# Kernel optimization log

Measured on AMD Instinct MI355X. Metric: run time of the kernel, lower is better.

The kernel has to match this reference:

```python
import jax, jax.numpy as jnp
import numpy as np

N = 50000   # nodes
E = 800000  # edges
IN = 128    # in_channels
H = 256     # hidden_channels
G = 128     # graphs in batch
NEG_SLOPE = 0.2


def _gat_conv(x, src, dst, W, a_src, a_dst, b):
    # PyG GATConv, heads=1: xp = W x; e_ij = LeakyReLU(a_src.xp_j + a_dst.xp_i);
    # softmax over incoming edges of target i; out_i = sum_j alpha_ij xp_j + b
    xp = x @ W                                   # [N, H]
    e = jax.nn.leaky_relu(xp[src] @ a_src + xp[dst] @ a_dst, NEG_SLOPE)  # [Et]
    m = jax.ops.segment_max(e, dst, num_segments=N)
    m = jnp.where(jnp.isfinite(m), m, 0.0)
    p = jnp.exp(e - m[dst])
    denom = jax.ops.segment_sum(p, dst, num_segments=N)
    alpha = p / denom[dst]
    return jax.ops.segment_sum(alpha[:, None] * xp[src], dst, num_segments=N) + b


def _gru_step_h0(x, W_ih, W_hh, b_ih, b_hh):
    # torch.nn.GRU, seq_len=1, h0=0. Gate order: r, z, n.
    gi = x @ W_ih.T + b_ih                       # [N, 3H]
    i_r, i_z, i_n = jnp.split(gi, 3, axis=-1)
    h_r, h_z, h_n = jnp.split(b_hh, 3)           # h0=0 -> hidden gates are biases
    r = jax.nn.sigmoid(i_r + h_r)
    z = jax.nn.sigmoid(i_z + h_z)
    n = jnp.tanh(i_n + r * h_n)
    return (1.0 - z) * n                         # + z * h0 (=0)


def setup_inputs() -> dict:
    key = jax.random.key(0)
    ks = jax.random.split(key, 18)
    s = 0.05
    inp = {
        "x": jax.random.normal(ks[0], (N, IN), jnp.float32),
        "edge_index": jax.random.randint(ks[1], (2, E), 0, N, dtype=jnp.int32).astype(jnp.int64),
        "batch": jnp.sort(jax.random.randint(ks[2], (N,), 0, G, dtype=jnp.int32)).astype(jnp.int64),
        # GAT layer 0 (in->H) and layer 1 (H->H)
        "W0": jax.random.normal(ks[3], (IN, H), jnp.float32) * s,
        "a_src0": jax.random.normal(ks[4], (H,), jnp.float32) * s,
        "a_dst0": jax.random.normal(ks[5], (H,), jnp.float32) * s,
        "b0": jnp.zeros((H,), jnp.float32),
        "W1": jax.random.normal(ks[6], (H, H), jnp.float32) * s,
        "a_src1": jax.random.normal(ks[7], (H,), jnp.float32) * s,
        "a_dst1": jax.random.normal(ks[8], (H,), jnp.float32) * s,
        "b1": jnp.zeros((H,), jnp.float32),
        # GRU(H, H)
        "W_ih": jax.random.normal(ks[9], (3 * H, H), jnp.float32) * s,
        "W_hh": jax.random.normal(ks[10], (3 * H, H), jnp.float32) * s,
        "b_ih": jnp.zeros((3 * H,), jnp.float32),
        "b_hh": jnp.zeros((3 * H,), jnp.float32),
        # super_node_fc
        "Wf": jax.random.normal(ks[11], (H, H), jnp.float32) * s,
        "bf": jnp.zeros((H,), jnp.float32),
    }
    return inp


def reference(x, edge_index, batch, W0, a_src0, a_dst0, b0, W1, a_src1, a_dst1, b1,
              W_ih, W_hh, b_ih, b_hh, Wf, bf):
    # add self loops (PyG GATConv default)
    loops = jnp.arange(N, dtype=edge_index.dtype)
    src = jnp.concatenate([edge_index[0], loops])
    dst = jnp.concatenate([edge_index[1], loops])

    h = jax.nn.relu(_gat_conv(x, src, dst, W0, a_src0, a_dst0, b0))  # dropout=identity (eval)
    h = jax.nn.relu(_gat_conv(h, src, dst, W1, a_src1, a_dst1, b1))

    h = _gru_step_h0(h, W_ih, W_hh, b_ih, b_hh)                      # [N, H]

    h = jax.ops.segment_sum(h, batch, num_segments=G)                # global_add_pool [G, H]
    super_node = jnp.mean(h, axis=0, keepdims=True)                  # [1, H]
    super_node = jax.nn.relu(super_node @ Wf.T + bf)
    return jnp.concatenate([h, jnp.broadcast_to(super_node, (G, H))], axis=1)  # [G, 2H]
```

## Files before the change

kernel.cpp:

```cpp
#include <hip/hip_runtime.h>
#include <hip/hip_fp16.h>
#include <math.h>

#define N_NODES 50000
#define N_PAD   50176
#define N_EDGES 800000
#define ET (N_EDGES + N_NODES)
#define IN_CH 128
#define H 256
#define G_GRAPHS 128
#define NEG_SLOPE 0.2f
#define NB 391

typedef __attribute__((ext_vector_type(8))) short short8;
typedef __attribute__((ext_vector_type(4))) float f32x4;
typedef __attribute__((ext_vector_type(2))) float f32x2;
typedef unsigned short u16;
typedef unsigned char u8;


#if __has_builtin(__builtin_amdgcn_cvt_f32_fp8) && __has_builtin(__builtin_amdgcn_cvt_pk_fp8_f32)
#define USE_FP8_BUILTINS 1
#else
#define USE_FP8_BUILTINS 0
#endif
#if USE_FP8_BUILTINS && __has_builtin(__builtin_amdgcn_cvt_pk_f32_fp8)
#define HAVE_PK_DEC 1
#else
#define HAVE_PK_DEC 0
#endif

__device__ inline u16 f2bf(float v) {
    unsigned u = __float_as_uint(v);
    unsigned r = (u + 0x7FFFu + ((u >> 16) & 1u)) >> 16;
    return (u16)r;
}
__device__ inline float bf2f(u16 v) {
    return __uint_as_float(((unsigned)v) << 16);
}

#if USE_FP8_BUILTINS
#define FP8_WSCALE 1.0f
__device__ inline unsigned fp8_pack4(float a, float b, float c, float d) {
    int v = 0;
    v = __builtin_amdgcn_cvt_pk_fp8_f32(a, b, v, false);
    v = __builtin_amdgcn_cvt_pk_fp8_f32(c, d, v, true);
    return (unsigned)v;
}
__device__ inline void fp8_dec4(unsigned rv, float& f0, float& f1, float& f2, float& f3) {
#if HAVE_PK_DEC
    f32x2 lo = __builtin_amdgcn_cvt_pk_f32_fp8((int)rv, false);
    f32x2 hi = __builtin_amdgcn_cvt_pk_f32_fp8((int)rv, true);
    f0 = lo.x; f1 = lo.y; f2 = hi.x; f3 = hi.y;
#else
    f0 = __builtin_amdgcn_cvt_f32_fp8((int)rv, 0);
    f1 = __builtin_amdgcn_cvt_f32_fp8((int)rv, 1);
    f2 = __builtin_amdgcn_cvt_f32_fp8((int)rv, 2);
    f3 = __builtin_amdgcn_cvt_f32_fp8((int)rv, 3);
#endif
}
#else
#define FP8_WSCALE 256.0f
__device__ inline u8 fp8_enc1(float f) {
    unsigned u = __float_as_uint(f);
    unsigned s = (u >> 31) << 7;
    float a = fabsf(f);
    if (a >= 448.f) return (u8)(s | 0x7E);
    unsigned bits = __float_as_uint(a);
    int exp = (int)((bits >> 23) & 255) - 127;
    unsigned m23 = bits & 0x7fffff;
    if (exp < -6) {
        int m = (int)rintf(a * 512.f);
        if (m >= 8) return (u8)(s | (1 << 3));
        return (u8)(s | m);
    }
    int e8 = exp + 7;
    unsigned m = m23 >> 20, rem = m23 & 0xFFFFF;
    if (rem > 0x80000 || (rem == 0x80000 && (m & 1))) m++;
    if (m == 8) { m = 0; e8++; }
    if (e8 > 15 || (e8 == 15 && m == 7)) return (u8)(s | 0x7E);
    return (u8)(s | (e8 << 3) | m);
}
__device__ inline unsigned fp8_pack4(float a, float b, float c, float d) {
    return (unsigned)fp8_enc1(a) | ((unsigned)fp8_enc1(b) << 8) |
           ((unsigned)fp8_enc1(c) << 16) | ((unsigned)fp8_enc1(d) << 24);
}
__device__ inline void fp8_dec4(unsigned rv, float& f0, float& f1, float& f2, float& f3) {
    unsigned hA = ((rv & 0x00800080u) << 8) | ((rv & 0x007f007fu) << 7);
    unsigned rs = rv >> 8;
    unsigned hB = ((rs & 0x00800080u) << 8) | ((rs & 0x007f007fu) << 7);
    __half2 a = *(__half2*)&hA;
    __half2 b = *(__half2*)&hB;
    f0 = __low2float(a);  f2 = __high2float(a);
    f1 = __low2float(b);  f3 = __high2float(b);
}
#endif

__device__ inline void async_cp16(const u16* g, u16* l) {
    __builtin_amdgcn_global_load_lds(
        (const __attribute__((address_space(1))) unsigned int*)g,
        (__attribute__((address_space(3))) unsigned int*)l,
        16, 0, 0);
}

__global__ __launch_bounds__(256) void bucket_hist(const int* __restrict__ ei,
                                                   int* __restrict__ gcnt) {
    __shared__ int h[NB];
    int t = threadIdx.x;
    for (int b = t; b < NB; b += 256) h[b] = 0;
    __syncthreads();
    for (int e = blockIdx.x * 256 + t; e < N_EDGES; e += gridDim.x * 256)
        atomicAdd(&h[ei[N_EDGES + e] >> 7], 1);
    __syncthreads();
    for (int b = t; b < NB; b += 256)
        if (h[b]) atomicAdd(&gcnt[b], h[b]);
}

__global__ __launch_bounds__(512) void bucket_scan(const int* __restrict__ gcnt,
                                                   int* __restrict__ off,
                                                   int* __restrict__ cur) {
    __shared__ int s[NB + 1];
    int t = threadIdx.x;
    if (t < NB) s[t] = gcnt[t];
    __syncthreads();
    if (t == 0) {
        int a = 0;
        for (int b = 0; b < NB; b++) { int c = s[b]; s[b] = a; a += c; }
        s[NB] = a;
    }
    __syncthreads();
    if (t <= NB) { off[t] = s[t]; if (t < NB) cur[t] = s[t]; }
}

#define EPT 16
__global__ __launch_bounds__(256) void bucket_scatter(const int* __restrict__ ei,
                                                      int* __restrict__ bucketCur,
                                                      int2* __restrict__ rec) {
    __shared__ int cnt[NB];
    __shared__ int base[NB];
    int t = threadIdx.x;
    for (int b = t; b < NB; b += 256) cnt[b] = 0;
    __syncthreads();
    int e0 = blockIdx.x * (256 * EPT);
    int sa[EPT], da[EPT], rk[EPT];
#pragma unroll
    for (int k = 0; k < EPT; k++) {
        int e = e0 + k * 256 + t;
        if (e < N_EDGES) {
            sa[k] = ei[e];
            da[k] = ei[N_EDGES + e];
            rk[k] = atomicAdd(&cnt[da[k] >> 7], 1);
        }
    }
    __syncthreads();
    for (int b = t; b < NB; b += 256) {
        int c = cnt[b];
        base[b] = c ? atomicAdd(&bucketCur[b], c) : 0;
    }
    __syncthreads();
#pragma unroll
    for (int k = 0; k < EPT; k++) {
        int e = e0 + k * 256 + t;
        if (e < N_EDGES) rec[base[da[k] >> 7] + rk[k]] = make_int2(sa[k], da[k]);
    }
}

__global__ __launch_bounds__(256) void build_csr(const int2* __restrict__ rec,
                                                 const int* __restrict__ off,
                                                 int* __restrict__ indptr,
                                                 int* __restrict__ eidsSrc) {
    __shared__ int cnt[128];
    __shared__ int scn[128];
    __shared__ int cur[128];
    int b = blockIdx.x, t = threadIdx.x;
    int nInB = N_NODES - b * 128;
    if (nInB > 128) nInB = 128;
    if (t < 128) cnt[t] = 0;
    __syncthreads();
    int lo = off[b], hi = off[b + 1];
    for (int i = lo + t; i < hi; i += 256) atomicAdd(&cnt[rec[i].y & 127], 1);
    __syncthreads();
    if (t < 128) scn[t] = cnt[t] + 1;
    __syncthreads();
    for (int o = 1; o < 128; o <<= 1) {
        int v = 0;
        if (t < 128 && t >= o) v = scn[t - o];
        __syncthreads();
        if (t < 128 && t >= o) scn[t] += v;
        __syncthreads();
    }
    int base = off[b] + 128 * b;
    if (t < nInB) {
        int start = base + (t ? scn[t - 1] : 0);
        int node = b * 128 + t;
        indptr[node] = start;
        eidsSrc[start] = node;
        cur[t] = start + 1;
    }
    if (b == 0 && t == 0) indptr[N_NODES] = ET;
    __syncthreads();
    for (int i = lo + t; i < hi; i += 256) {
        int2 r = rec[i];
        int pos = atomicAdd(&cur[r.y & 127], 1);
        eidsSrc[pos] = r.x;
    }
}

__global__ __launch_bounds__(256) void prep_kernel(const float* __restrict__ x,
                                                   const float* __restrict__ Wih,
                                                   const float* __restrict__ W0,
                                                   const float* __restrict__ W1,
                                                   const float* __restrict__ b0,
                                                   const float* __restrict__ b1,
                                                   u16* __restrict__ x_bf,
                                                   u16* __restrict__ Wih_bf,
                                                   u16* __restrict__ W0t,
                                                   u16* __restrict__ W1t,
                                                   float* __restrict__ b0p,
                                                   float* __restrict__ b1p) {
    int i = blockIdx.x * 256 + threadIdx.x;
    int seg = blockIdx.y;
    if (seg == 0) {
        if (i < N_NODES * IN_CH / 4) {
            float4 v = *(const float4*)&x[i * 4];
            ushort4 o = {f2bf(v.x), f2bf(v.y), f2bf(v.z), f2bf(v.w)};
            *(ushort4*)&x_bf[i * 4] = o;
        }
    } else if (seg == 1) {
        if (i < 3 * H * H) {
            int r = i >> 8, p = i & 255;
            int c = ((p & 15) << 4) | (p >> 4);
            Wih_bf[(size_t)r * H + p] = f2bf(Wih[(size_t)r * H + c]);
        }
    } else if (seg == 2) {
        if (i < IN_CH * H) {
            int k = i / H, n = i % H;
            W0t[(size_t)n * IN_CH + k] = f2bf(W0[i]);
        }
    } else if (seg == 3) {
        if (i < H * H) {
            int n = i >> 8, p = i & 255;
            int c = ((p & 15) << 4) | (p >> 4);
            W1t[(size_t)n * H + p] = f2bf(W1[(size_t)c * H + n]);
        }
    } else {
        if (i < H) {
            int c = ((i & 15) << 4) | (i >> 4);
            b0p[i] = b0[c];
            b1p[i] = b1[c];
        }
    }
}

template <bool FUSE>
__global__ __launch_bounds__(256, 2) void gemm_wide(const u16* __restrict__ A,
                                                    const u16* __restrict__ Bt,
                                                    u16* __restrict__ C,
                                                    u8* __restrict__ C8,
                                                    const float* __restrict__ avS,
                                                    const float* __restrict__ avD,
                                                    float* __restrict__ sS,
                                                    float* __restrict__ sD,
                                                    int M, int K, int Ntot) {
    __shared__ u16 As[128][32];
    __shared__ u16 Bs[256][32];
    __shared__ float rSp[2][128];
    __shared__ float rDp[2][128];
    int t = threadIdx.x;
    int m0 = blockIdx.x * 128;
    int n0 = blockIdx.y * 256;
    int wave = t >> 6, lane = t & 63;
    int wm = (wave >> 1) * 64, wn = (wave & 1) * 128;
    int lrow = lane & 15;
    int lq = lane >> 4;

    f32x4 acc[4][8];
#pragma unroll
    for (int i = 0; i < 4; i++)
#pragma unroll
        for (int j = 0; j < 8; j++)
            acc[i][j] = (f32x4){0.f, 0.f, 0.f, 0.f};

    int r0 = t >> 2;
    int qs = (t & 3) ^ ((t >> 3) & 3);
    const u16* gA0 = A + (size_t)(m0 + r0) * K + qs * 8;
    const u16* gA1 = gA0 + (size_t)64 * K;
    const u16* gB0 = Bt + (size_t)(n0 + r0) * K + qs * 8;
    const u16* gB1 = gB0 + (size_t)64 * K;
    const u16* gB2 = gB0 + (size_t)128 * K;
    const u16* gB3 = gB0 + (size_t)192 * K;
    u16* lA0 = &As[0][0] + t * 8;
    u16* lA1 = lA0 + 256 * 8;
    u16* lB0 = &Bs[0][0] + t * 8;
    u16* lB1 = lB0 + 256 * 8;
    u16* lB2 = lB0 + 512 * 8;
    u16* lB3 = lB0 + 768 * 8;

    int swz8 = (lq ^ ((lrow >> 1) & 3)) * 8;

    for (int k0 = 0; k0 < K; k0 += 32) {
        __syncthreads();
        async_cp16(gA0 + k0, lA0);
        async_cp16(gA1 + k0, lA1);
        async_cp16(gB0 + k0, lB0);
        async_cp16(gB1 + k0, lB1);
        async_cp16(gB2 + k0, lB2);
        async_cp16(gB3 + k0, lB3);
        __syncthreads();
        short8 af[4], bfr[8];
#pragma unroll
        for (int i = 0; i < 4; i++)
            af[i] = *(const short8*)&As[wm + i * 16 + lrow][swz8];
#pragma unroll
        for (int j = 0; j < 8; j++)
            bfr[j] = *(const short8*)&Bs[wn + j * 16 + lrow][swz8];
#pragma unroll
        for (int i = 0; i < 4; i++)
#pragma unroll
            for (int j = 0; j < 8; j++)
                acc[i][j] = __builtin_amdgcn_mfma_f32_16x16x32_bf16(af[i], bfr[j], acc[i][j], 0, 0, 0);
    }

    if constexpr (FUSE) {
        float aS[8], aD[8];
#pragma unroll
        for (int j = 0; j < 8; j++) {
            aS[j] = avS[wn + j * 16 + lrow];
            aD[j] = avD[wn + j * 16 + lrow];
        }
        int woff = wn ? 8 : 0;
#pragma unroll
        for (int i = 0; i < 4; i++) {
#pragma unroll
            for (int reg = 0; reg < 4; reg++) {
                float ps = 0.f, pd = 0.f;
#pragma unroll
                for (int j = 0; j < 8; j++) {
                    float v = acc[i][j][reg];
                    ps += v * aS[j];
                    pd += v * aD[j];
                }
                uint2 pk;
                pk.x = fp8_pack4(acc[i][0][reg], acc[i][1][reg], acc[i][2][reg], acc[i][3][reg]);
                pk.y = fp8_pack4(acc[i][4][reg], acc[i][5][reg], acc[i][6][reg], acc[i][7][reg]);
                int row = m0 + wm + i * 16 + lq * 4 + reg;
                *(uint2*)&C8[(size_t)row * 256 + lrow * 16 + woff] = pk;
#pragma unroll
                for (int msk = 1; msk < 16; msk <<= 1) {
                    ps += __shfl_xor(ps, msk);
                    pd += __shfl_xor(pd, msk);
                }
                if (lrow == 0) {
                    int lr = wm + i * 16 + lq * 4 + reg;
                    rSp[wave & 1][lr] = ps;
                    rDp[wave & 1][lr] = pd;
                }
            }
        }
        __syncthreads();
        if (t < 128) {
            int gm = m0 + t;
            if (gm < M) {
                sS[gm] = rSp[0][t] + rSp[1][t];
                sD[gm] = rDp[0][t] + rDp[1][t];
            }
        }
    } else {
#pragma unroll
        for (int i = 0; i < 4; i++) {
#pragma unroll
            for (int reg = 0; reg < 4; reg++) {
                int gm = m0 + wm + i * 16 + lq * 4 + reg;
                if (gm < M) {
#pragma unroll
                    for (int j = 0; j < 8; j++) {
                        int gn = n0 + wn + j * 16 + lrow;
                        C[(size_t)gm * Ntot + gn] = f2bf(acc[i][j][reg]);
                    }
                }
            }
        }
    }
}

__global__ __launch_bounds__(256) void gat_agg_fp8(const u8* __restrict__ xp8,
                                                   const float* __restrict__ s_src,
                                                   const float* __restrict__ s_dst,
                                                   const int* __restrict__ indptr,
                                                   const int* __restrict__ eidsSrc,
                                                   const float* __restrict__ bias,
                                                   u16* __restrict__ out) {
    __shared__ int2 sSW[4][64];
    int wave = threadIdx.x >> 6, lane = threadIdx.x & 63;
    int n = blockIdx.x * 4 + wave;
    int start = indptr[n];
    int deg = indptr[n + 1] - start;
    float sdn = s_dst[n];
    int col = lane << 2;
    float a0 = 0.f, a1 = 0.f, a2 = 0.f, a3 = 0.f;

    if (deg <= 64) {
        int s = 0;
        float v = -1e30f;
        if (lane < deg) {
            s = eidsSrc[start + lane];
            float u = s_src[s] + sdn;
            v = (u >= 0.f) ? u : NEG_SLOPE * u;
        }
        float m = v;
#pragma unroll
        for (int off = 32; off; off >>= 1) m = fmaxf(m, __shfl_xor(m, off));
        float pw = (lane < deg) ? expf(v - m) : 0.f;
        float dsum = pw;
#pragma unroll
        for (int off = 32; off; off >>= 1) dsum += __shfl_xor(dsum, off);
        float w = pw * (FP8_WSCALE / dsum);
        sSW[wave][lane] = make_int2(s * H, __float_as_int(w));
        int j = 0;
        for (; j + 16 <= deg; j += 16) {
            unsigned rv[16];
            float wv[16];
#pragma unroll
            for (int k = 0; k < 16; k++) {
                int2 sw = sSW[wave][j + k];
                wv[k] = __int_as_float(sw.y);
                rv[k] = *(const unsigned*)&xp8[(size_t)(unsigned)sw.x + col];
            }
#pragma unroll
            for (int k = 0; k < 16; k++) {
                float f0, f1, f2, f3;
                fp8_dec4(rv[k], f0, f1, f2, f3);
                a0 += wv[k] * f0; a1 += wv[k] * f1;
                a2 += wv[k] * f2; a3 += wv[k] * f3;
            }
        }
        if (j + 8 <= deg) {
            unsigned rv[8];
            float wv[8];
#pragma unroll
            for (int k = 0; k < 8; k++) {
                int2 sw = sSW[wave][j + k];
                wv[k] = __int_as_float(sw.y);
                rv[k] = *(const unsigned*)&xp8[(size_t)(unsigned)sw.x + col];
            }
#pragma unroll
            for (int k = 0; k < 8; k++) {
                float f0, f1, f2, f3;
                fp8_dec4(rv[k], f0, f1, f2, f3);
                a0 += wv[k] * f0; a1 += wv[k] * f1;
                a2 += wv[k] * f2; a3 += wv[k] * f3;
            }
            j += 8;
        }
        for (; j < deg; j++) {
            int2 sw = sSW[wave][j];
            float wj = __int_as_float(sw.y);
            unsigned rv = *(const unsigned*)&xp8[(size_t)(unsigned)sw.x + col];
            float f0, f1, f2, f3;
            fp8_dec4(rv, f0, f1, f2, f3);
            a0 += wj * f0; a1 += wj * f1; a2 += wj * f2; a3 += wj * f3;
        }
    } else {
        float m = -1e30f;
        for (int i = lane; i < deg; i += 64) {
            int s = eidsSrc[start + i];
            float u = s_src[s] + sdn;
            u = (u >= 0.f) ? u : NEG_SLOPE * u;
            m = fmaxf(m, u);
        }
#pragma unroll
        for (int off = 32; off; off >>= 1) m = fmaxf(m, __shfl_xor(m, off));
        float dsum = 0.f;
        for (int i = lane; i < deg; i += 64) {
            int s = eidsSrc[start + i];
            float u = s_src[s] + sdn;
            u = (u >= 0.f) ? u : NEG_SLOPE * u;
            dsum += expf(u - m);
        }
#pragma unroll
        for (int off = 32; off; off >>= 1) dsum += __shfl_xor(dsum, off);
        float dinv = FP8_WSCALE / dsum;
        for (int base = 0; base < deg; base += 64) {
            int cnt = min(64, deg - base);
            int s = 0; float w = 0.f;
            if (lane < cnt) {
                s = eidsSrc[start + base + lane];
                float u = s_src[s] + sdn;
                u = (u >= 0.f) ? u : NEG_SLOPE * u;
                w = expf(u - m) * dinv;
            }
            sSW[wave][lane] = make_int2(s * H, __float_as_int(w));
            for (int j = 0; j < cnt; j++) {
                int2 sw = sSW[wave][j];
                float wj = __int_as_float(sw.y);
                unsigned rv = *(const unsigned*)&xp8[(size_t)(unsigned)sw.x + col];
                float f0, f1, f2, f3;
                fp8_dec4(rv, f0, f1, f2, f3);
                a0 += wj * f0; a1 += wj * f1; a2 += wj * f2; a3 += wj * f3;
            }
        }
    }
    float4 bv = *(const float4*)&bias[col];
    ushort4 o;
    o.x = f2bf(fmaxf(a0 + bv.x, 0.f));
    o.y = f2bf(fmaxf(a1 + bv.y, 0.f));
    o.z = f2bf(fmaxf(a2 + bv.z, 0.f));
    o.w = f2bf(fmaxf(a3 + bv.w, 0.f));
    *(ushort4*)&out[(size_t)n * H + col] = o;
}

__global__ __launch_bounds__(256) void gru_gates_pool(const u16* __restrict__ gates,
                                                      const float* __restrict__ b_ih,
                                                      const float* __restrict__ b_hh,
                                                      const int* __restrict__ batch,
                                                      float* __restrict__ pooled) {
    int t = threadIdx.x;
    int i0 = blockIdx.x * 16;
    if (i0 >= N_NODES) return;
    float bir = b_ih[t], biz = b_ih[256 + t], bin_ = b_ih[512 + t];
    float bhr = b_hh[t], bhz = b_hh[256 + t], bhn = b_hh[512 + t];
    int iend = min(16, N_NODES - i0);
    float acc = 0.f;
    int cur_g = batch[i0];
    for (int i = 0; i < iend; i++) {
        size_t row = (size_t)(i0 + i) * 768;
        float ir = bf2f(gates[row + t]);
        float iz = bf2f(gates[row + 256 + t]);
        float in_ = bf2f(gates[row + 512 + t]);
        float r = 1.f / (1.f + expf(-(ir + bir + bhr)));
        float z = 1.f / (1.f + expf(-(iz + biz + bhz)));
        float nn = tanhf(in_ + bin_ + r * bhn);
        float h = (1.f - z) * nn;
        int g = batch[i0 + i];
        if (g != cur_g) {
            atomicAdd(&pooled[(size_t)cur_g * H + t], acc);
            acc = 0.f;
            cur_g = g;
        }
        acc += h;
    }
    atomicAdd(&pooled[(size_t)cur_g * H + t], acc);
}

__global__ __launch_bounds__(256) void super_kernel(const float* __restrict__ pooled,
                                                    const float* __restrict__ Wf,
                                                    const float* __restrict__ bf,
                                                    float* __restrict__ sup) {
    __shared__ float smean[256];
    int t = threadIdx.x;
    float s = 0.f;
    for (int g = 0; g < G_GRAPHS; g++) s += pooled[(size_t)g * H + t];
    smean[t] = s / (float)G_GRAPHS;
    __syncthreads();
    float acc = 0.f;
    for (int k = 0; k < H; k++) acc += smean[k] * Wf[(size_t)t * H + k];
    acc += bf[t];
    sup[t] = fmaxf(acc, 0.f);
}

__global__ __launch_bounds__(256) void writeout(const float* __restrict__ pooled,
                                                const float* __restrict__ sup,
                                                float* __restrict__ out) {
    int idx = blockIdx.x * 256 + threadIdx.x;
    int g = idx >> 9, c = idx & 511;
    out[idx] = (c < H) ? pooled[(size_t)g * H + c] : sup[c - H];
}

extern "C" void kernel_launch(void* const* d_in, const int* in_sizes, int n_in,
                              void* d_out, int out_size, void* d_ws, size_t ws_size,
                              hipStream_t stream) {
    const float* x      = (const float*)d_in[0];
    const int*   ei     = (const int*)d_in[1];
    const int*   batch  = (const int*)d_in[2];
    const float* W0     = (const float*)d_in[3];
    const float* a_src0 = (const float*)d_in[4];
    const float* a_dst0 = (const float*)d_in[5];
    const float* b0     = (const float*)d_in[6];
    const float* W1     = (const float*)d_in[7];
    const float* a_src1 = (const float*)d_in[8];
    const float* a_dst1 = (const float*)d_in[9];
    const float* b1     = (const float*)d_in[10];
    const float* W_ih   = (const float*)d_in[11];
    const float* b_ih   = (const float*)d_in[13];
    const float* b_hh   = (const float*)d_in[14];
    const float* Wf     = (const float*)d_in[15];
    const float* bf     = (const float*)d_in[16];
    float* out = (float*)d_out;

    char* p = (char*)d_ws;
    auto alloc = [&](size_t bytes) -> void* {
        void* r = (void*)p;
        p += (bytes + 255) & ~(size_t)255;
        return r;
    };
    u16*   h_bf   = (u16*)alloc((size_t)N_PAD * H * 2);
    u16*   x_bf   = (u16*)alloc((size_t)N_PAD * IN_CH * 2);
    u8*    xp8    = (u8*)alloc((size_t)N_PAD * H);
    u16*   gatesC = (u16*)alloc((size_t)N_PAD * 3 * H * 2);
    u16*   W0t    = (u16*)alloc((size_t)H * IN_CH * 2);
    u16*   W1t    = (u16*)alloc((size_t)H * H * 2);
    u16*   Wih_bf = (u16*)alloc((size_t)3 * H * H * 2);
    float* b0p    = (float*)alloc((size_t)H * 4);
    float* b1p    = (float*)alloc((size_t)H * 4);
    float* s_src  = (float*)alloc((size_t)N_NODES * 4);
    float* s_dst  = (float*)alloc((size_t)N_NODES * 4);
    int2*  rec    = (int2*)alloc((size_t)N_EDGES * 8);
    int*   eidsSrc= (int*)alloc((size_t)ET * 4);
    int*   indptr = (int*)alloc((size_t)(N_NODES + 1) * 4);
    int*   gBkt   = (int*)alloc((size_t)(NB + 1) * 4);
    int*   bktOff = (int*)alloc((size_t)(NB + 1) * 4);
    int*   bktCur = (int*)alloc((size_t)(NB + 1) * 4);
    float* pooled = (float*)alloc((size_t)G_GRAPHS * H * 4);
    float* sup    = (float*)alloc((size_t)H * 4);

    hipMemsetAsync(gBkt, 0, (size_t)NB * 4, stream);
    bucket_hist<<<NB, 256, 0, stream>>>(ei, gBkt);
    bucket_scan<<<1, 512, 0, stream>>>(gBkt, bktOff, bktCur);
    bucket_scatter<<<(N_EDGES + 256 * EPT - 1) / (256 * EPT), 256, 0, stream>>>(ei, bktCur, rec);
    build_csr<<<NB, 256, 0, stream>>>(rec, bktOff, indptr, eidsSrc);

    prep_kernel<<<dim3((N_NODES * IN_CH / 4 + 255) / 256, 5), 256, 0, stream>>>(
        x, W_ih, W0, W1, b0, b1, x_bf, Wih_bf, W0t, W1t, b0p, b1p);

    const int MB = (N_NODES + 127) / 128;
    const int WB = N_NODES / 4;
    gemm_wide<true><<<dim3(MB, 1), 256, 0, stream>>>(
        x_bf, W0t, nullptr, xp8, a_src0, a_dst0, s_src, s_dst, N_NODES, IN_CH, H);
    gat_agg_fp8<<<WB, 256, 0, stream>>>(xp8, s_src, s_dst, indptr, eidsSrc, b0p, h_bf);
    gemm_wide<true><<<dim3(MB, 1), 256, 0, stream>>>(
        h_bf, W1t, nullptr, xp8, a_src1, a_dst1, s_src, s_dst, N_NODES, H, H);
    gat_agg_fp8<<<WB, 256, 0, stream>>>(xp8, s_src, s_dst, indptr, eidsSrc, b1p, h_bf);
    hipMemsetAsync(pooled, 0, (size_t)G_GRAPHS * H * 4, stream);
    gemm_wide<false><<<dim3(MB, 3), 256, 0, stream>>>(
        h_bf, Wih_bf, gatesC, nullptr, nullptr, nullptr, nullptr, nullptr, N_NODES, H, 3 * H);
    gru_gates_pool<<<(N_NODES + 15) / 16, 256, 0, stream>>>(gatesC, b_ih, b_hh, batch, pooled);
    super_kernel<<<1, 256, 0, stream>>>(pooled, Wf, bf, sup);
    writeout<<<(G_GRAPHS * 2 * H) / 256, 256, 0, stream>>>(pooled, sup, out);
}
```

Baseline: 337.9 us.

## Precompute per-edge attention logits in separate kernel; widen GEMM K-tile to 64

Adds a dst array to the CSR build and a new edge_lv kernel that computes the LeakyReLU attention logit per edge into a contiguous buffer. The aggregation kernel then reads these logits directly instead of gathering s_src randomly in up to three passes per node. Separately, the GEMM K tile is doubled from 32 to 64, with a new swizzle, to halve the number of barrier-separated load stages. The cost is an extra kernel launch and an extra ET-sized read/write per layer, plus twice the LDS per GEMM block, which may reduce occupancy.

```diff
diff --git a/kernel.cpp b/kernel.cpp
--- a/kernel.cpp
+++ b/kernel.cpp
@@ -168,7 +168,8 @@
 __global__ __launch_bounds__(256) void build_csr(const int2* __restrict__ rec,
                                                  const int* __restrict__ off,
                                                  int* __restrict__ indptr,
-                                                 int* __restrict__ eidsSrc) {
+                                                 int* __restrict__ eidsSrc,
+                                                 int* __restrict__ dstA) {
     __shared__ int cnt[128];
     __shared__ int scn[128];
     __shared__ int cur[128];
@@ -195,6 +196,7 @@
         int node = b * 128 + t;
         indptr[node] = start;
         eidsSrc[start] = node;
+        dstA[start] = node;
         cur[t] = start + 1;
     }
     if (b == 0 && t == 0) indptr[N_NODES] = ET;
@@ -203,6 +205,7 @@
         int2 r = rec[i];
         int pos = atomicAdd(&cur[r.y & 127], 1);
         eidsSrc[pos] = r.x;
+        dstA[pos] = r.y;
     }
 }
 
@@ -262,8 +265,8 @@
                                                     float* __restrict__ sS,
                                                     float* __restrict__ sD,
                                                     int M, int K, int Ntot) {
-    __shared__ u16 As[128][32];
-    __shared__ u16 Bs[256][32];
+    __shared__ u16 As[128][64];
+    __shared__ u16 Bs[256][64];
     __shared__ float rSp[2][128];
     __shared__ float rDp[2][128];
     int t = threadIdx.x;
@@ -281,44 +284,42 @@
         for (int j = 0; j < 8; j++)
             acc[i][j] = (f32x4){0.f, 0.f, 0.f, 0.f};
 
-    int r0 = t >> 2;
-    int qs = (t & 3) ^ ((t >> 3) & 3);
-    const u16* gA0 = A + (size_t)(m0 + r0) * K + qs * 8;
-    const u16* gA1 = gA0 + (size_t)64 * K;
-    const u16* gB0 = Bt + (size_t)(n0 + r0) * K + qs * 8;
-    const u16* gB1 = gB0 + (size_t)64 * K;
-    const u16* gB2 = gB0 + (size_t)128 * K;
-    const u16* gB3 = gB0 + (size_t)192 * K;
-    u16* lA0 = &As[0][0] + t * 8;
-    u16* lA1 = lA0 + 256 * 8;
-    u16* lB0 = &Bs[0][0] + t * 8;
-    u16* lB1 = lB0 + 256 * 8;
-    u16* lB2 = lB0 + 512 * 8;
-    u16* lB3 = lB0 + 768 * 8;
-
-    int swz8 = (lq ^ ((lrow >> 1) & 3)) * 8;
-
-    for (int k0 = 0; k0 < K; k0 += 32) {
+    int rowc = t >> 3;
+    int sq = t & 7;
+    int qg = (((sq >> 2) ^ (rowc & 1)) << 2) | ((sq & 3) ^ ((rowc >> 1) & 3));
+    const u16* pA = A + (size_t)(m0 + rowc) * K + qg * 8;
+    const u16* pB = Bt + (size_t)(n0 + rowc) * K + qg * 8;
+    u16* lA = &As[0][0] + t * 8;
+    u16* lB = &Bs[0][0] + t * 8;
+
+    int swzlow = lq ^ ((lrow >> 1) & 3);
+    int pbit = (lrow & 1) << 2;
+
+    for (int k0 = 0; k0 < K; k0 += 64) {
         __syncthreads();
-        async_cp16(gA0 + k0, lA0);
-        async_cp16(gA1 + k0, lA1);
-        async_cp16(gB0 + k0, lB0);
-        async_cp16(gB1 + k0, lB1);
-        async_cp16(gB2 + k0, lB2);
-        async_cp16(gB3 + k0, lB3);
+#pragma unroll
+        for (int m = 0; m < 4; m++)
+            async_cp16(pA + (size_t)32 * m * K + k0, lA + 2048 * m);
+#pragma unroll
+        for (int m = 0; m < 8; m++)
+            async_cp16(pB + (size_t)32 * m * K + k0, lB + 2048 * m);
         __syncthreads();
-        short8 af[4], bfr[8];
-#pragma unroll
-        for (int i = 0; i < 4; i++)
-            af[i] = *(const short8*)&As[wm + i * 16 + lrow][swz8];
-#pragma unroll
-        for (int j = 0; j < 8; j++)
-            bfr[j] = *(const short8*)&Bs[wn + j * 16 + lrow][swz8];
-#pragma unroll
-        for (int i = 0; i < 4; i++)
+#pragma unroll
+        for (int h = 0; h < 2; h++) {
+            int colh = (((h << 2) ^ pbit) | swzlow) * 8;
+            short8 af[4], bfr[8];
+#pragma unroll
+            for (int i = 0; i < 4; i++)
+                af[i] = *(const short8*)&As[wm + i * 16 + lrow][colh];
 #pragma unroll
             for (int j = 0; j < 8; j++)
-                acc[i][j] = __builtin_amdgcn_mfma_f32_16x16x32_bf16(af[i], bfr[j], acc[i][j], 0, 0, 0);
+                bfr[j] = *(const short8*)&Bs[wn + j * 16 + lrow][colh];
+#pragma unroll
+            for (int i = 0; i < 4; i++)
+#pragma unroll
+                for (int j = 0; j < 8; j++)
+                    acc[i][j] = __builtin_amdgcn_mfma_f32_16x16x32_bf16(af[i], bfr[j], acc[i][j], 0, 0, 0);
+        }
     }
 
     if constexpr (FUSE) {
@@ -383,9 +384,20 @@
     }
 }
 
+__global__ __launch_bounds__(256) void edge_lv(const int* __restrict__ eidsSrc,
+                                               const int* __restrict__ dstA,
+                                               const float* __restrict__ s_src,
+                                               const float* __restrict__ s_dst,
+                                               float* __restrict__ lv) {
+    int i = blockIdx.x * 256 + threadIdx.x;
+    if (i < ET) {
+        float u = s_src[eidsSrc[i]] + s_dst[dstA[i]];
+        lv[i] = (u >= 0.f) ? u : NEG_SLOPE * u;
+    }
+}
+
 __global__ __launch_bounds__(256) void gat_agg_fp8(const u8* __restrict__ xp8,
-                                                   const float* __restrict__ s_src,
-                                                   const float* __restrict__ s_dst,
+                                                   const float* __restrict__ lv,
                                                    const int* __restrict__ indptr,
                                                    const int* __restrict__ eidsSrc,
                                                    const float* __restrict__ bias,
@@ -395,7 +407,6 @@
     int n = blockIdx.x * 4 + wave;
     int start = indptr[n];
     int deg = indptr[n + 1] - start;
-    float sdn = s_dst[n];
     int col = lane << 2;
     float a0 = 0.f, a1 = 0.f, a2 = 0.f, a3 = 0.f;
 
@@ -404,8 +415,7 @@
         float v = -1e30f;
         if (lane < deg) {
             s = eidsSrc[start + lane];
-            float u = s_src[s] + sdn;
-            v = (u >= 0.f) ? u : NEG_SLOPE * u;
+            v = lv[start + lane];
         }
         float m = v;
 #pragma unroll
@@ -462,21 +472,13 @@
         }
     } else {
         float m = -1e30f;
-        for (int i = lane; i < deg; i += 64) {
-            int s = eidsSrc[start + i];
-            float u = s_src[s] + sdn;
-            u = (u >= 0.f) ? u : NEG_SLOPE * u;
-            m = fmaxf(m, u);
-        }
+        for (int i = lane; i < deg; i += 64)
+            m = fmaxf(m, lv[start + i]);
 #pragma unroll
         for (int off = 32; off; off >>= 1) m = fmaxf(m, __shfl_xor(m, off));
         float dsum = 0.f;
-        for (int i = lane; i < deg; i += 64) {
-            int s = eidsSrc[start + i];
-            float u = s_src[s] + sdn;
-            u = (u >= 0.f) ? u : NEG_SLOPE * u;
-            dsum += expf(u - m);
-        }
+        for (int i = lane; i < deg; i += 64)
+            dsum += expf(lv[start + i] - m);
 #pragma unroll
         for (int off = 32; off; off >>= 1) dsum += __shfl_xor(dsum, off);
         float dinv = FP8_WSCALE / dsum;
@@ -485,9 +487,7 @@
             int s = 0; float w = 0.f;
             if (lane < cnt) {
                 s = eidsSrc[start + base + lane];
-                float u = s_src[s] + sdn;
-                u = (u >= 0.f) ? u : NEG_SLOPE * u;
-                w = expf(u - m) * dinv;
+                w = expf(lv[start + base + lane] - m) * dinv;
             }
             sSW[wave][lane] = make_int2(s * H, __float_as_int(w));
             for (int j = 0; j < cnt; j++) {
@@ -604,8 +604,10 @@
     float* b1p    = (float*)alloc((size_t)H * 4);
     float* s_src  = (float*)alloc((size_t)N_NODES * 4);
     float* s_dst  = (float*)alloc((size_t)N_NODES * 4);
+    float* lv     = (float*)alloc((size_t)ET * 4);
     int2*  rec    = (int2*)alloc((size_t)N_EDGES * 8);
     int*   eidsSrc= (int*)alloc((size_t)ET * 4);
+    int*   dstA   = (int*)alloc((size_t)ET * 4);
     int*   indptr = (int*)alloc((size_t)(N_NODES + 1) * 4);
     int*   gBkt   = (int*)alloc((size_t)(NB + 1) * 4);
     int*   bktOff = (int*)alloc((size_t)(NB + 1) * 4);
@@ -617,19 +619,22 @@
     bucket_hist<<<NB, 256, 0, stream>>>(ei, gBkt);
     bucket_scan<<<1, 512, 0, stream>>>(gBkt, bktOff, bktCur);
     bucket_scatter<<<(N_EDGES + 256 * EPT - 1) / (256 * EPT), 256, 0, stream>>>(ei, bktCur, rec);
-    build_csr<<<NB, 256, 0, stream>>>(rec, bktOff, indptr, eidsSrc);
+    build_csr<<<NB, 256, 0, stream>>>(rec, bktOff, indptr, eidsSrc, dstA);
 
     prep_kernel<<<dim3((N_NODES * IN_CH / 4 + 255) / 256, 5), 256, 0, stream>>>(
         x, W_ih, W0, W1, b0, b1, x_bf, Wih_bf, W0t, W1t, b0p, b1p);
 
     const int MB = (N_NODES + 127) / 128;
     const int WB = N_NODES / 4;
+    const int EB = (ET + 255) / 256;
     gemm_wide<true><<<dim3(MB, 1), 256, 0, stream>>>(
         x_bf, W0t, nullptr, xp8, a_src0, a_dst0, s_src, s_dst, N_NODES, IN_CH, H);
-    gat_agg_fp8<<<WB, 256, 0, stream>>>(xp8, s_src, s_dst, indptr, eidsSrc, b0p, h_bf);
+    edge_lv<<<EB, 256, 0, stream>>>(eidsSrc, dstA, s_src, s_dst, lv);
+    gat_agg_fp8<<<WB, 256, 0, stream>>>(xp8, lv, indptr, eidsSrc, b0p, h_bf);
     gemm_wide<true><<<dim3(MB, 1), 256, 0, stream>>>(
         h_bf, W1t, nullptr, xp8, a_src1, a_dst1, s_src, s_dst, N_NODES, H, H);
-    gat_agg_fp8<<<WB, 256, 0, stream>>>(xp8, s_src, s_dst, indptr, eidsSrc, b1p, h_bf);
+    edge_lv<<<EB, 256, 0, stream>>>(eidsSrc, dstA, s_src, s_dst, lv);
+    gat_agg_fp8<<<WB, 256, 0, stream>>>(xp8, lv, indptr, eidsSrc, b1p, h_bf);
     hipMemsetAsync(pooled, 0, (size_t)G_GRAPHS * H * 4, stream);
     gemm_wide<false><<<dim3(MB, 3), 256, 0, stream>>>(
         h_bf, Wih_bf, gatesC, nullptr, nullptr, nullptr, nullptr, nullptr, N_NODES, H, 3 * H);
```

After: 341.1 us. Within noise of the previous version (+0.9%).
